# Kernel tuning notes

Measured on AMD Instinct MI355X. Metric: run time of the kernel, lower is better.

## Reference

```python
import jax, jax.numpy as jnp
import numpy as np

SIGMA_SPATIAL = 1.0
SIGMA_BILATERAL = 0.25
RADIUS = 1
PATCH = 2 * RADIUS + 1  # 3


def _spatial_kernel():
    x, y = np.mgrid[-RADIUS:RADIUS + 1, -RADIUS:RADIUS + 1]
    w1 = np.exp(-(x ** 2 + y ** 2) / (2.0 * SIGMA_SPATIAL ** 2))
    return jnp.asarray(w1.reshape(-1), dtype=jnp.float32)  # [PATCH*PATCH]


def _extract_patches(x):
    # x: [B,H,W,C] -> [B,H,W,PATCH*PATCH,C] via reflect-padded shifted slices
    B, H, W, C = x.shape
    xp = jnp.pad(x, ((0, 0), (RADIUS, RADIUS), (RADIUS, RADIUS), (0, 0)), mode='reflect')
    return jnp.stack(
        [xp[:, dy:dy + H, dx:dx + W, :] for dy in range(PATCH) for dx in range(PATCH)],
        axis=3,
    )


def setup_inputs() -> dict:
    key = jax.random.key(0)
    k1, k2 = jax.random.split(key)
    src = jax.random.uniform(k1, (2, 512, 512, 21), dtype=jnp.float32)
    im = jax.random.uniform(k2, (2, 512, 512, 3), dtype=jnp.float32)
    return {"src": src, "im": im}


def reference(src, im):
    w1 = _spatial_kernel()  # [9]
    im_patches = _extract_patches(im)                      # [B,H,W,9,Ci]
    diff2 = jnp.sum((im_patches - im[:, :, :, None, :]) ** 2, axis=-1)  # [B,H,W,9]
    w = jnp.exp(-diff2 / (2.0 * SIGMA_BILATERAL ** 2)) * w1            # [B,H,W,9]
    src_patches = _extract_patches(src)                    # [B,H,W,9,Cs]
    num = jnp.sum(src_patches * w[..., None], axis=3)      # [B,H,W,Cs]
    den = jnp.sum(w, axis=3, keepdims=True)                # [B,H,W,1]
    return num / den
```

## Files before the change

### kernel.cpp

```cpp
#include <hip/hip_runtime.h>

#define BATCH 2
#define H 512
#define W 512
#define CS 21
#define CI 3
#define P 128
#define R 8
#define TPB 256
#define GROWS (R + 2)
#define GSL (P + 2)
#define GSZ (GROWS * GSL * CI)
#define NSETS (R * P)
#define SWF (NSETS * 12)

typedef float f32x4 __attribute__((ext_vector_type(4)));

__device__ __forceinline__ void fma4(float4& a, const float4 v, const float w) {
    a.x = fmaf(v.x, w, a.x);
    a.y = fmaf(v.y, w, a.y);
    a.z = fmaf(v.z, w, a.z);
    a.w = fmaf(v.w, w, a.w);
}

__device__ __forceinline__ void nt_store4(float* p, const float4 v) {
    __builtin_nontemporal_store(*(const f32x4*)&v, (f32x4*)p);
}

#define LOAD3(dst, rr, om, oc, op)                              \
    (dst)[0] = *(const float4*)(srow[rr] + (om));               \
    (dst)[1] = *(const float4*)(srow[rr] + (oc));               \
    (dst)[2] = *(const float4*)(srow[rr] + (op));

#define VA_I(r) ((r) < 6 ? (r) : 5)
#define VB_I(r) ((r) < 6 ? 0 : (r) - 6)
#define VR(va, vb, r, k) ((r) < 6 ? (va)[VA_I(r)][(k)] : (vb)[VB_I(r)][(k)])

#define COMPUTE8(va, vb, px, oc)                                             \
    {                                                                        \
        _Pragma("unroll")                                                    \
        for (int j = 0; j < R; ++j) {                                        \
            const float* wd = &s_u[((j << 7) + (px)) * 12];                  \
            float4 wA = *(const float4*)(wd + 0);                            \
            float4 wB = *(const float4*)(wd + 4);                            \
            float  w8 = wd[8];                                               \
            float4 acc = {0.f, 0.f, 0.f, 0.f};                               \
            fma4(acc, VR(va, vb, j + 0, 0), wA.x);                           \
            fma4(acc, VR(va, vb, j + 0, 1), wA.y);                           \
            fma4(acc, VR(va, vb, j + 0, 2), wA.z);                           \
            fma4(acc, VR(va, vb, j + 1, 0), wA.w);                           \
            fma4(acc, VR(va, vb, j + 1, 1), wB.x);                           \
            fma4(acc, VR(va, vb, j + 1, 2), wB.y);                           \
            fma4(acc, VR(va, vb, j + 2, 0), wB.z);                           \
            fma4(acc, VR(va, vb, j + 2, 1), wB.w);                           \
            fma4(acc, VR(va, vb, j + 2, 2), w8);                             \
            nt_store4(ob + (size_t)j * rs + (oc), acc);                      \
        }                                                                    \
    }

__global__ __launch_bounds__(TPB, 3) void jbu_kernel(
    const float* __restrict__ src, const float* __restrict__ im,
    float* __restrict__ out)
{
    __shared__ __align__(16) float s_u[SWF];

    const int t = threadIdx.x;

    const int f      = blockIdx.x;
    const int xcd    = f & 7;
    const int g      = f >> 3;
    const int rowgrp = (xcd << 3) | (g & 7);
    const int rem    = g >> 3;
    const int x0     = (rem & 3) << 7;
    const int b      = rem >> 2;
    const int y0     = rowgrp << 3;

    const size_t rs = (size_t)W * CS;
    const float* sb = src + (size_t)b * H * rs;
    const float* srow[GROWS];
    #pragma unroll
    for (int rr = 0; rr < GROWS; ++rr) {
        int v = y0 - 1 + rr;
        int tyr = (v < 0) ? 1 : ((v >= H) ? 2 * H - 2 - v : v);
        srow[rr] = sb + (size_t)tyr * rs + (size_t)x0 * CS;
    }

    const int px0   = t / 6;
    const int q0    = t - px0 * 6;
    const int coff0 = (q0 == 5) ? 17 : (q0 << 2);
    const int x_    = x0 + px0;
    const int xm_   = (x_ == 0)     ? 1     : x_ - 1;
    const int xp_   = (x_ == W - 1) ? W - 2 : x_ + 1;
    const int om0   = (xm_ - x0) * CS + coff0;
    const int oc0   = px0 * CS + coff0;
    const int op0   = (xp_ - x0) * CS + coff0;

    float4 va0[6][3];
    #pragma unroll
    for (int rr = 0; rr < 6; ++rr) { LOAD3(va0[rr], rr, om0, oc0, op0) }

    const float* imb = im + (size_t)b * (H * W * CI);
    for (int i = t; i < GSZ; i += TPB) {
        int rr   = i / (GSL * CI);
        int remi = i - rr * (GSL * CI);
        int slot = remi / CI;
        int ch   = remi - slot * CI;
        int gx   = x0 + slot - 1;
        gx = (gx < 0) ? 1 : ((gx >= W) ? W - 2 : gx);
        int vv = y0 - 1 + rr;
        int tyr = (vv < 0) ? 1 : ((vv >= H) ? 2 * H - 2 - vv : vv);
        const float* gsrc = imb + ((size_t)tyr * W + gx) * CI + ch;
        __builtin_amdgcn_global_load_lds(
            (const __attribute__((address_space(1))) void*)gsrc,
            (__attribute__((address_space(3))) void*)(s_u + i), 4, 0, 0);
    }
    __syncthreads();

    float wreg[4][9];
    {
        const float w1k[9] = {0.36787944f, 0.60653066f, 0.36787944f,
                              0.60653066f, 1.0f,        0.60653066f,
                              0.36787944f, 0.60653066f, 0.36787944f};
        #pragma unroll
        for (int ii = 0; ii < 4; ++ii) {
            int idx = ii * TPB + t;
            int r   = idx >> 7;
            int px  = idx & (P - 1);
            int cb  = ((r + 1) * GSL + px + 1) * CI;
            float c0 = s_u[cb + 0], c1 = s_u[cb + 1], c2 = s_u[cb + 2];
            float wv[9];
            float den = 0.f;
            #pragma unroll
            for (int k = 0; k < 9; ++k) {
                int dy = k / 3, dx = k % 3;
                int ib = ((r + dy) * GSL + px + dx) * CI;
                float d0 = s_u[ib + 0] - c0;
                float d1 = s_u[ib + 1] - c1;
                float d2 = s_u[ib + 2] - c2;
                float w = __expf(-8.0f * (d0 * d0 + d1 * d1 + d2 * d2)) * w1k[k];
                wv[k] = w;
                den += w;
            }
            float inv = 1.0f / den;
            #pragma unroll
            for (int k = 0; k < 9; ++k) wreg[ii][k] = wv[k] * inv;
        }
    }
    __syncthreads();

    #pragma unroll
    for (int ii = 0; ii < 4; ++ii) {
        int idx = ii * TPB + t;
        float* wd = &s_u[idx * 12];
        *(float4*)(wd + 0) = make_float4(wreg[ii][0], wreg[ii][1], wreg[ii][2], wreg[ii][3]);
        *(float4*)(wd + 4) = make_float4(wreg[ii][4], wreg[ii][5], wreg[ii][6], wreg[ii][7]);
        wd[8] = wreg[ii][8];
    }
    __syncthreads();

    float* ob = out + ((size_t)(b * H + y0)) * rs + (size_t)x0 * CS;

    {
        float4 vb0[4][3];
        #pragma unroll
        for (int rr = 0; rr < 4; ++rr) { LOAD3(vb0[rr], rr + 6, om0, oc0, op0) }
        COMPUTE8(va0, vb0, px0, oc0)
    }

    #pragma unroll
    for (int it = 1; it < (P * 6) / TPB; ++it) {
        const int item = it * TPB + t;
        const int px   = item / 6;
        const int q    = item - px * 6;
        const int coff = (q == 5) ? 17 : (q << 2);
        const int x    = x0 + px;
        const int xm   = (x == 0)     ? 1     : x - 1;
        const int xp   = (x == W - 1) ? W - 2 : x + 1;
        const int om   = (xm - x0) * CS + coff;
        const int oc   = px * CS + coff;
        const int op   = (xp - x0) * CS + coff;

        float4 va[6][3];
        #pragma unroll
        for (int rr = 0; rr < 6; ++rr) { LOAD3(va[rr], rr, om, oc, op) }
        float4 vb[4][3];
        #pragma unroll
        for (int rr = 0; rr < 4; ++rr) { LOAD3(vb[rr], rr + 6, om, oc, op) }
        COMPUTE8(va, vb, px, oc)
    }
}

extern "C" void kernel_launch(void* const* d_in, const int* in_sizes, int n_in,
                              void* d_out, int out_size, void* d_ws, size_t ws_size,
                              hipStream_t stream) {
    const float* src = (const float*)d_in[0];
    const float* im  = (const float*)d_in[1];
    float* out = (float*)d_out;
    dim3 grid((W / P) * (H / R) * BATCH, 1, 1);
    jbu_kernel<<<grid, TPB, 0, stream>>>(src, im, out);
}
```

Before: 103.9 us.

## Halve tile width to 64 pixels and split weight LDS into separate buffers

Tile width drops from 128 to 64 pixels, doubling the grid and giving 384 work items per 256-thread block, so the second pass runs only on a partial set of threads. Weights move from a reused staging buffer into dedicated shared arrays (wA, wB, w8). This drops one barrier and the register staging copy between weight compute and write-back. The aim is more blocks for latency hiding and less sync. The cost is more halo re-reads of src and im, plus idle threads in the tail pass.

```diff
diff --git a/kernel.cpp b/kernel.cpp
--- a/kernel.cpp
+++ b/kernel.cpp
@@ -5,14 +5,14 @@
 #define W 512
 #define CS 21
 #define CI 3
-#define P 128
+#define P 64
 #define R 8
 #define TPB 256
 #define GROWS (R + 2)
 #define GSL (P + 2)
 #define GSZ (GROWS * GSL * CI)
 #define NSETS (R * P)
-#define SWF (NSETS * 12)
+#define NITEMS (P * 6)
 
 typedef float f32x4 __attribute__((ext_vector_type(4)));
 
@@ -40,10 +40,10 @@
     {                                                                        \
         _Pragma("unroll")                                                    \
         for (int j = 0; j < R; ++j) {                                        \
-            const float* wd = &s_u[((j << 7) + (px)) * 12];                  \
-            float4 wA = *(const float4*)(wd + 0);                            \
-            float4 wB = *(const float4*)(wd + 4);                            \
-            float  w8 = wd[8];                                               \
+            const int s = (j << 6) + (px);                                   \
+            float4 wA = *(const float4*)&s_wA[s * 4];                        \
+            float4 wB = *(const float4*)&s_wB[s * 4];                        \
+            float  w8 = s_w8[s];                                             \
             float4 acc = {0.f, 0.f, 0.f, 0.f};                               \
             fma4(acc, VR(va, vb, j + 0, 0), wA.x);                           \
             fma4(acc, VR(va, vb, j + 0, 1), wA.y);                           \
@@ -62,7 +62,10 @@
     const float* __restrict__ src, const float* __restrict__ im,
     float* __restrict__ out)
 {
-    __shared__ __align__(16) float s_u[SWF];
+    __shared__ float s_g[GSZ];
+    __shared__ __align__(16) float s_wA[NSETS * 4];
+    __shared__ __align__(16) float s_wB[NSETS * 4];
+    __shared__ float s_w8[NSETS];
 
     const int t = threadIdx.x;
 
@@ -71,8 +74,8 @@
     const int g      = f >> 3;
     const int rowgrp = (xcd << 3) | (g & 7);
     const int rem    = g >> 3;
-    const int x0     = (rem & 3) << 7;
-    const int b      = rem >> 2;
+    const int x0     = (rem & 7) << 6;
+    const int b      = rem >> 3;
     const int y0     = rowgrp << 3;
 
     const size_t rs = (size_t)W * CS;
@@ -112,49 +115,39 @@
         const float* gsrc = imb + ((size_t)tyr * W + gx) * CI + ch;
         __builtin_amdgcn_global_load_lds(
             (const __attribute__((address_space(1))) void*)gsrc,
-            (__attribute__((address_space(3))) void*)(s_u + i), 4, 0, 0);
+            (__attribute__((address_space(3))) void*)(s_g + i), 4, 0, 0);
     }
     __syncthreads();
 
-    float wreg[4][9];
     {
         const float w1k[9] = {0.36787944f, 0.60653066f, 0.36787944f,
                               0.60653066f, 1.0f,        0.60653066f,
                               0.36787944f, 0.60653066f, 0.36787944f};
         #pragma unroll
-        for (int ii = 0; ii < 4; ++ii) {
+        for (int ii = 0; ii < NSETS / TPB; ++ii) {
             int idx = ii * TPB + t;
-            int r   = idx >> 7;
+            int r   = idx >> 6;
             int px  = idx & (P - 1);
             int cb  = ((r + 1) * GSL + px + 1) * CI;
-            float c0 = s_u[cb + 0], c1 = s_u[cb + 1], c2 = s_u[cb + 2];
+            float c0 = s_g[cb + 0], c1 = s_g[cb + 1], c2 = s_g[cb + 2];
             float wv[9];
             float den = 0.f;
             #pragma unroll
             for (int k = 0; k < 9; ++k) {
                 int dy = k / 3, dx = k % 3;
                 int ib = ((r + dy) * GSL + px + dx) * CI;
-                float d0 = s_u[ib + 0] - c0;
-                float d1 = s_u[ib + 1] - c1;
-                float d2 = s_u[ib + 2] - c2;
+                float d0 = s_g[ib + 0] - c0;
+                float d1 = s_g[ib + 1] - c1;
+                float d2 = s_g[ib + 2] - c2;
                 float w = __expf(-8.0f * (d0 * d0 + d1 * d1 + d2 * d2)) * w1k[k];
                 wv[k] = w;
                 den += w;
             }
             float inv = 1.0f / den;
-            #pragma unroll
-            for (int k = 0; k < 9; ++k) wreg[ii][k] = wv[k] * inv;
+            *(float4*)&s_wA[idx * 4] = make_float4(wv[0] * inv, wv[1] * inv, wv[2] * inv, wv[3] * inv);
+            *(float4*)&s_wB[idx * 4] = make_float4(wv[4] * inv, wv[5] * inv, wv[6] * inv, wv[7] * inv);
+            s_w8[idx] = wv[8] * inv;
         }
-    }
-    __syncthreads();
-
-    #pragma unroll
-    for (int ii = 0; ii < 4; ++ii) {
-        int idx = ii * TPB + t;
-        float* wd = &s_u[idx * 12];
-        *(float4*)(wd + 0) = make_float4(wreg[ii][0], wreg[ii][1], wreg[ii][2], wreg[ii][3]);
-        *(float4*)(wd + 4) = make_float4(wreg[ii][4], wreg[ii][5], wreg[ii][6], wreg[ii][7]);
-        wd[8] = wreg[ii][8];
     }
     __syncthreads();
 
@@ -167,9 +160,8 @@
         COMPUTE8(va0, vb0, px0, oc0)
     }
 
-    #pragma unroll
-    for (int it = 1; it < (P * 6) / TPB; ++it) {
-        const int item = it * TPB + t;
+    if (t < NITEMS - TPB) {
+        const int item = TPB + t;
         const int px   = item / 6;
         const int q    = item - px * 6;
         const int coff = (q == 5) ? 17 : (q << 2);
```

Result: no change. 102.7 us (-1.2%).
